# Performance work log

Hardware: AMD Instinct MI355X
Metric: run time of the kernel (lower is better)

## Reference

```python
import jax, jax.numpy as jnp
import numpy as np

B, S, H, NH, K = 8, 1024, 1024, 16, 512
HD = H // NH  # head dim = 64


def setup_inputs() -> dict:
    key = jax.random.key(0)
    ks = jax.random.split(key, 9)
    hidden_states = jax.random.normal(ks[0], (B, S, H), jnp.float32)
    # remain_layers: exactly K nonzero entries per row (static max_tokens = K)
    scores = jax.random.uniform(ks[1], (B, S))
    thresh = jnp.sort(scores, axis=1)[:, S - K][:, None]
    remain_layers = (scores >= thresh).astype(jnp.int32)
    attention_mask = jnp.zeros((B, 1, 1, S), jnp.float32)  # additive mask
    init = 0.02
    Wq = jax.random.normal(ks[2], (H, H), jnp.float32) * init
    bq = jnp.zeros((H,), jnp.float32)
    Wk = jax.random.normal(ks[3], (H, H), jnp.float32) * init
    bk = jnp.zeros((H,), jnp.float32)
    Wv = jax.random.normal(ks[4], (H, H), jnp.float32) * init
    bv = jnp.zeros((H,), jnp.float32)
    return {"hidden_states": hidden_states, "attention_mask": attention_mask,
            "remain_layers": remain_layers, "Wq": Wq, "bq": bq,
            "Wk": Wk, "bk": bk, "Wv": Wv, "bv": bv}


def _heads(x):  # [B, L, H] -> [B, NH, L, HD]
    b, l, _ = x.shape
    return x.reshape(b, l, NH, HD).transpose(0, 2, 1, 3)


def reference(hidden_states, attention_mask, remain_layers, Wq, bq, Wk, bk, Wv, bv):
    # get_reduced_hidden: per-row gather of tokens with remain_layers > 0,
    # in original position order, zero-padded to max_tokens (= K here).
    order = jnp.argsort(1 - remain_layers, axis=1, stable=True)  # nonzeros first, order kept
    idx = order[:, :K]                                           # [B, K]
    reduced = jnp.take_along_axis(hidden_states, idx[:, :, None], axis=1)  # [B, K, H]
    valid = (jnp.take_along_axis(remain_layers, idx, axis=1) > 0)
    reduced = reduced * valid[:, :, None].astype(reduced.dtype)  # zero-pad slots

    q = _heads(reduced @ Wq.T + bq)          # [B, NH, K, HD]
    k = _heads(hidden_states @ Wk.T + bk)    # [B, NH, S, HD]
    v = _heads(hidden_states @ Wv.T + bv)    # [B, NH, S, HD]

    scores = jnp.einsum('bhqd,bhkd->bhqk', q, k) / np.sqrt(HD).astype(np.float32)
    scores = scores + attention_mask         # additive mask broadcast
    probs = jax.nn.softmax(scores, axis=-1)  # dropout is identity at eval
    ctx = jnp.einsum('bhqk,bhkd->bhqd', probs, v)  # [B, NH, K, HD]
    ctx = ctx.transpose(0, 2, 1, 3).reshape(B, K, H)
    return ctx
```

## Files before the change

### kernel.cpp

```cpp
#include <hip/hip_runtime.h>
#include <hip/hip_bf16.h>
#include <stdint.h>

#define S_LEN 1024
#define HDIM  1024
#define NHEADS 16
#define HEAD_D 64
#define KSEL  512
#define BATCH 8

typedef unsigned short ushort_t;
typedef __attribute__((ext_vector_type(8))) __bf16 bf16x8;
typedef __attribute__((ext_vector_type(4))) float  f32x4;
typedef __attribute__((ext_vector_type(16))) float f32x16;

typedef const __attribute__((address_space(1))) void cg_void;
typedef __attribute__((address_space(3))) void lds_void;

__device__ __forceinline__ void gl_lds16(const void* g, void* l) {
    __builtin_amdgcn_global_load_lds((cg_void*)g, (lds_void*)l, 16, 0, 0);
}

__device__ __forceinline__ ushort_t f2bf(float f) {
    union { float f; unsigned int i; } x; x.f = f;
    unsigned int r = (x.i + 0x7fffu + ((x.i >> 16) & 1u)) >> 16;
    return (ushort_t)r;
}

#define BAR() __asm__ volatile("s_barrier" ::: "memory")
#define VMCNT(n) __asm__ volatile("s_waitcnt vmcnt(" #n ")" ::: "memory")
#define LGKM0() __asm__ volatile("s_waitcnt lgkmcnt(0)" ::: "memory")

__global__ __launch_bounds__(1024) void prep_kernel(
    const float* __restrict__ hidden, const float* __restrict__ wq,
    const float* __restrict__ wk, const float* __restrict__ wv,
    const int* __restrict__ remain,
    ushort_t* __restrict__ hbf, ushort_t* __restrict__ wqb,
    ushort_t* __restrict__ wkb, ushort_t* __restrict__ wvb,
    int* __restrict__ idx, int* __restrict__ valid) {
    __shared__ int wsum[16];
    __shared__ int woff[17];
    int blk = blockIdx.x;
    if (blk < 2816) {
        const float* s; ushort_t* d; int base;
        if (blk < 2048)      { s = hidden; d = hbf; base = blk; }
        else if (blk < 2304) { s = wq; d = wqb; base = blk - 2048; }
        else if (blk < 2560) { s = wk; d = wkb; base = blk - 2304; }
        else                 { s = wv; d = wvb; base = blk - 2560; }
        int i = base * 1024 + threadIdx.x;
        float4 v = ((const float4*)s)[i];
        ushort4 o;
        o.x = f2bf(v.x); o.y = f2bf(v.y); o.z = f2bf(v.z); o.w = f2bf(v.w);
        ((ushort4*)d)[i] = o;
    } else {
        int b = blk - 2816, t = threadIdx.x;
        int r = remain[b * S_LEN + t];
        unsigned long long m = __ballot(r != 0);
        int lane = t & 63, w = t >> 6;
        int pre = __popcll(m & ((1ull << lane) - 1ull));
        if (lane == 0) wsum[w] = __popcll(m);
        __syncthreads();
        if (t == 0) { int a = 0; for (int i = 0; i < 16; i++) { woff[i] = a; a += wsum[i]; } woff[16] = a; }
        __syncthreads();
        int tot = woff[16];
        int onesBefore = woff[w] + pre;
        int slot = r ? onesBefore : (tot + (t - onesBefore));
        if (slot < KSEL) { idx[b * KSEL + slot] = t; valid[b * KSEL + slot] = r; }
    }
}

#define QSCALE 0.1803368801111244f
#define LT_PITCH 136
__global__ __launch_bounds__(256, 4) void gemm_fused(
    const ushort_t* __restrict__ hbf, const ushort_t* __restrict__ wkv,
    const ushort_t* __restrict__ wq,
    const float* __restrict__ bk, const float* __restrict__ bv,
    const float* __restrict__ bq,
    const int* __restrict__ idx, const int* __restrict__ valid,
    ushort_t* __restrict__ kp, ushort_t* __restrict__ vt, ushort_t* __restrict__ qp) {
    __shared__ __align__(16) ushort_t pool[16384];
    ushort_t* As = pool;
    ushort_t* Bs = pool + 8192;
    const int i = blockIdx.x;
    int z, bmI, bnI;
    if (i < 256) { z = 1; bmI = i >> 3; bnI = i & 7; }
    else         { z = 0; int ii = i - 256; int x = ii & 7, j = ii >> 3;
                   bmI = x * 8 + (j & 7); bnI = j >> 3; }
    const long bm = (long)bmI * 128;
    const int bn = bnI * 128;

    const int tid = threadIdx.x;
    const int lane = tid & 63;
    const int w = tid >> 6;
    const int quad = lane >> 4;
    const int cl = lane & 15;
    const int srow = w * 16 + (lane >> 2);
    const int fs = ((lane >> 2) & 3) ^ ((lane >> 4) & 3);
    const int scol = ((lane & 3) ^ fs) * 8;
    const int lds_off = w * 512 + lane * 8;
    const int wr = (w >> 1) * 64, wc = (w & 1) * 64;
    const int fr = (cl & 3) ^ ((cl >> 2) & 3);
    const int qo = (quad ^ fr) * 8;

    const ushort_t* W = z ? wq : wkv;

    long ab[2];
#pragma unroll
    for (int p = 0; p < 2; p++) {
        long gr = bm + p * 64 + srow;
        if (z == 0) ab[p] = gr * HDIM;
        else {
            int b_ = (int)(gr >> 9);
            int src = idx[(b_ << 9) + ((int)gr & 511)];
            ab[p] = ((long)(b_ << 10) + src) * HDIM;
        }
    }

    f32x4 acc[4][4] = {};

    for (int k0 = 0; k0 < HDIM; k0 += 64) {
#pragma unroll
        for (int p = 0; p < 2; p++)
#pragma unroll
            for (int hh = 0; hh < 2; hh++) {
                gl_lds16(hbf + ab[p] + k0 + hh * 32 + scol, &As[hh * 4096 + p * 2048 + lds_off]);
                gl_lds16(W + ((long)(bn + p * 64 + srow)) * HDIM + k0 + hh * 32 + scol,
                         &Bs[hh * 4096 + p * 2048 + lds_off]);
            }
        __syncthreads();
#pragma unroll
        for (int hh = 0; hh < 2; hh++) {
            bf16x8 af[4], bfr[4];
#pragma unroll
            for (int mt = 0; mt < 4; mt++)
                af[mt] = *(const bf16x8*)&As[hh * 4096 + (wr + mt * 16 + cl) * 32 + qo];
#pragma unroll
            for (int nt = 0; nt < 4; nt++)
                bfr[nt] = *(const bf16x8*)&Bs[hh * 4096 + (wc + nt * 16 + cl) * 32 + qo];
#pragma unroll
            for (int mt = 0; mt < 4; mt++)
#pragma unroll
                for (int nt = 0; nt < 4; nt++)
                    acc[mt][nt] = __builtin_amdgcn_mfma_f32_16x16x32_bf16(af[mt], bfr[nt], acc[mt][nt], 0, 0, 0);
        }
        __syncthreads();
    }

    if (z == 1) {
#pragma unroll
        for (int nt = 0; nt < 4; nt++) {
            int col = bn + wc + nt * 16 + cl;
            float bvq = bq[col];
#pragma unroll
            for (int mt = 0; mt < 4; mt++) {
                long row = bm + wr + mt * 16 + quad * 4;
#pragma unroll
                for (int r = 0; r < 4; r++) {
                    float vm = (float)valid[row + r];
                    qp[(row + r) * HDIM + col] = f2bf((acc[mt][nt][r] * vm + bvq) * QSCALE);
                }
            }
        }
    } else if (bn < 1024) {
#pragma unroll
        for (int nt = 0; nt < 4; nt++) {
            int col = bn + wc + nt * 16 + cl;
            float bvk = bk[col];
#pragma unroll
            for (int mt = 0; mt < 4; mt++) {
                long row = bm + wr + mt * 16 + quad * 4;
#pragma unroll
                for (int r = 0; r < 4; r++)
                    kp[(row + r) * HDIM + col] = f2bf(acc[mt][nt][r] + bvk);
            }
        }
    } else {
        ushort_t* Lt = pool;
        long b_ = bm >> 10, s0 = bm & 1023;
#pragma unroll
        for (int p2 = 0; p2 < 2; p2++) {
            if ((w & 1) == p2) {
#pragma unroll
                for (int nt = 0; nt < 4; nt++) {
                    int cloc = nt * 16 + cl;
                    float bvv = bv[bn - 1024 + p2 * 64 + cloc];
#pragma unroll
                    for (int mt = 0; mt < 4; mt++) {
                        int row0 = wr + mt * 16 + quad * 4;
#pragma unroll
                        for (int r = 0; r < 4; r++)
                            Lt[cloc * LT_PITCH + row0 + r] = f2bf(acc[mt][nt][r] + bvv);
                    }
                }
            }
            __syncthreads();
            int c2 = tid >> 2, quarter = tid & 3;
            long gbase = ((b_ << 10) + (bn - 1024) + p2 * 64 + c2) * 1024 + s0 + quarter * 32;
            const ushort_t* src = Lt + c2 * LT_PITCH + quarter * 32;
#pragma unroll
            for (int q8 = 0; q8 < 4; q8++)
                *(bf16x8*)(vt + gbase + q8 * 8) = *(const bf16x8*)(src + q8 * 8);
            __syncthreads();
        }
    }
}

__global__ __launch_bounds__(256, 2) void attn_kernel(
    const ushort_t* __restrict__ qp, const ushort_t* __restrict__ kp,
    const ushort_t* __restrict__ vt, const float* __restrict__ mask,
    float* __restrict__ out) {
    __shared__ __align__(16) ushort_t ks[3][4096];
    __shared__ __align__(16) ushort_t vs[3][4096];
    __shared__ float mlds[1024];
    const int tid = threadIdx.x;
    const int lane = tid & 63;
    const int w = tid >> 6;
    const int ql = lane & 31;
    const int hi = lane >> 5;
    const int qt = blockIdx.x, h = blockIdx.y, b = blockIdx.z;

    const int sr2 = tid >> 3;
    const int scS = ((tid & 7) ^ (sr2 & 7)) * 8;
    const int dOf = tid * 8;

    const long kbase = (long)b * S_LEN;
    const long vbase = (long)b * 1024 + h * HEAD_D;

    {
        float4 mv4 = *(const float4*)(mask + b * S_LEN + tid * 4);
        mlds[tid * 4 + 0] = mv4.x * 1.44269504f;
        mlds[tid * 4 + 1] = mv4.y * 1.44269504f;
        mlds[tid * 4 + 2] = mv4.z * 1.44269504f;
        mlds[tid * 4 + 3] = mv4.w * 1.44269504f;
    }

    const long qrow0 = (long)b * KSEL + qt * 128 + w * 32;
    bf16x8 aq[4];
#pragma unroll
    for (int kd = 0; kd < 4; kd++)
        aq[kd] = *(const bf16x8*)(qp + (qrow0 + ql) * HDIM + h * HEAD_D + kd * 16 + hi * 8);

    f32x16 O[2] = {};
    float l_loc = 0.f;

    auto stage = [&](int t, int slot) {
#pragma unroll
        for (int j = 0; j < 2; j++) {
            gl_lds16(kp + (kbase + t * 64 + j * 32 + sr2) * (long)HDIM + h * HEAD_D + scS,
                     &ks[slot][j * 2048 + dOf]);
            gl_lds16(vt + (vbase + j * 32 + sr2) * (long)S_LEN + t * 64 + scS,
                     &vs[slot][j * 2048 + dOf]);
        }
    };

    stage(0, 0);
    stage(1, 1);
    LGKM0();

    int slotC = 0;
    int slotP = 2;
    for (int c = 0; c < S_LEN / 64; c++) {
        BAR();
        if (c + 2 < S_LEN / 64) stage(c + 2, slotP);
        if (c < 14)       { VMCNT(8); }
        else if (c == 14) { VMCNT(4); }
        else              { VMCNT(0); }
        BAR();
        const ushort_t* kb_ = ks[slotC];
        const ushort_t* vb_ = vs[slotC];

        f32x16 sc[2] = {};
        __builtin_amdgcn_s_setprio(1);
#pragma unroll
        for (int kd = 0; kd < 4; kd++)
#pragma unroll
            for (int mtk = 0; mtk < 2; mtk++) {
                int row = mtk * 32 + ql;
                bf16x8 af = *(const bf16x8*)&kb_[row * 64 + (((kd * 2 + hi) ^ (row & 7)) * 8)];
                sc[mtk] = __builtin_amdgcn_mfma_f32_32x32x16_bf16(af, aq[kd], sc[mtk], 0, 0, 0);
            }
        __builtin_amdgcn_s_setprio(0);

#pragma unroll
        for (int mtk = 0; mtk < 2; mtk++)
#pragma unroll
            for (int g = 0; g < 4; g++) {
                f32x4 m4 = *(const f32x4*)&mlds[c * 64 + mtk * 32 + g * 8 + hi * 4];
#pragma unroll
                for (int j = 0; j < 4; j++) {
                    float p_ = __builtin_amdgcn_exp2f(sc[mtk][g * 4 + j] + m4[j]);
                    sc[mtk][g * 4 + j] = p_;
                    l_loc += p_;
                }
            }

        bf16x8 pa[4];
#pragma unroll
        for (int mtk = 0; mtk < 2; mtk++)
#pragma unroll
            for (int sub = 0; sub < 2; sub++) {
                unsigned a0, a1, b0, b1;
                __asm__("v_cvt_pk_bf16_f32 %0, %1, %2" : "=v"(a0)
                        : "v"(sc[mtk][sub * 8 + 0]), "v"(sc[mtk][sub * 8 + 1]));
                __asm__("v_cvt_pk_bf16_f32 %0, %1, %2" : "=v"(a1)
                        : "v"(sc[mtk][sub * 8 + 2]), "v"(sc[mtk][sub * 8 + 3]));
                __asm__("v_cvt_pk_bf16_f32 %0, %1, %2" : "=v"(b0)
                        : "v"(sc[mtk][sub * 8 + 4]), "v"(sc[mtk][sub * 8 + 5]));
                __asm__("v_cvt_pk_bf16_f32 %0, %1, %2" : "=v"(b1)
                        : "v"(sc[mtk][sub * 8 + 6]), "v"(sc[mtk][sub * 8 + 7]));
                __asm__("v_permlane32_swap_b32 %0, %1" : "+v"(a0), "+v"(b0));
                __asm__("v_permlane32_swap_b32 %0, %1" : "+v"(a1), "+v"(b1));
                union { unsigned u[4]; bf16x8 v; } fr;
                fr.u[0] = a0; fr.u[1] = a1; fr.u[2] = b0; fr.u[3] = b1;
                pa[mtk * 2 + sub] = fr.v;
            }

        __builtin_amdgcn_s_setprio(1);
#pragma unroll
        for (int ks_ = 0; ks_ < 4; ks_++)
#pragma unroll
            for (int ntd = 0; ntd < 2; ntd++) {
                int row = ntd * 32 + ql;
                bf16x8 bvf = *(const bf16x8*)&vb_[row * 64 + (((ks_ * 2 + hi) ^ (row & 7)) * 8)];
                O[ntd] = __builtin_amdgcn_mfma_f32_32x32x16_bf16(bvf, pa[ks_], O[ntd], 0, 0, 0);
            }
        __builtin_amdgcn_s_setprio(0);

        slotC = (slotC == 2) ? 0 : slotC + 1;
        slotP = (slotP == 2) ? 0 : slotP + 1;
    }

    l_loc += __shfl_xor(l_loc, 32, 64);

#pragma unroll
    for (int ntd = 0; ntd < 2; ntd++)
#pragma unroll
        for (int g = 0; g < 4; g++) {
            float4 o4;
            o4.x = O[ntd][g * 4 + 0] / l_loc;
            o4.y = O[ntd][g * 4 + 1] / l_loc;
            o4.z = O[ntd][g * 4 + 2] / l_loc;
            o4.w = O[ntd][g * 4 + 3] / l_loc;
            *(float4*)(out + (qrow0 + ql) * HDIM + h * HEAD_D + ntd * 32 + g * 8 + hi * 4) = o4;
        }
}

extern "C" void kernel_launch(void* const* d_in, const int* in_sizes, int n_in,
                              void* d_out, int out_size, void* d_ws, size_t ws_size,
                              hipStream_t stream) {
    const float* hidden = (const float*)d_in[0];
    const float* mask   = (const float*)d_in[1];
    const int*   remain = (const int*)d_in[2];
    const float* Wq = (const float*)d_in[3];
    const float* bq = (const float*)d_in[4];
    const float* Wk = (const float*)d_in[5];
    const float* bk = (const float*)d_in[6];
    const float* Wv = (const float*)d_in[7];
    const float* bv = (const float*)d_in[8];
    float* out = (float*)d_out;

    char* ws = (char*)d_ws;
    size_t off = 0;
    int* idx   = (int*)(ws + off); off += 16384;
    int* valid = (int*)(ws + off); off += 16384;
    ushort_t* hbf = (ushort_t*)(ws + off); off += (size_t)BATCH * S_LEN * HDIM * 2;
    ushort_t* wqb = (ushort_t*)(ws + off); off += (size_t)HDIM * HDIM * 2;
    ushort_t* wkb = (ushort_t*)(ws + off); off += (size_t)HDIM * HDIM * 2;
    ushort_t* wvb = (ushort_t*)(ws + off); off += (size_t)HDIM * HDIM * 2;
    ushort_t* qp  = (ushort_t*)(ws + off); off += (size_t)BATCH * KSEL * HDIM * 2;
    ushort_t* kp  = (ushort_t*)(ws + off); off += (size_t)BATCH * S_LEN * HDIM * 2;
    ushort_t* vt  = (ushort_t*)(ws + off); off += (size_t)BATCH * S_LEN * HDIM * 2;

    prep_kernel<<<2824, 1024, 0, stream>>>(hidden, Wq, Wk, Wv, remain,
                                           hbf, wqb, wkb, wvb, idx, valid);
    gemm_fused<<<1280, 256, 0, stream>>>(hbf, wkb, wqb, bk, bv, bq,
                                         idx, valid, kp, vt, qp);
    attn_kernel<<<dim3(4, NHEADS, BATCH), 256, 0, stream>>>(qp, kp, vt, mask, out);
}
```

Measured before the change: 187.1 us.

## Split fused QKV GEMM into separate launches and remap attention blocks per XCD

The fused Q/K/V projection kernel is split into a dedicated Q GEMM and a K/V GEMM launched in two halves. This removes per-block branching on the Q path and the idx indirection from K/V blocks. The attention grid becomes 1D, with block IDs remapped so that the four query tiles of the same (batch, head) land on the same XCD and share K/V in its L2. The cost is extra kernel launches and smaller grids that may underfill the device.

```diff
diff --git a/kernel.cpp b/kernel.cpp
--- a/kernel.cpp
+++ b/kernel.cpp
@@ -71,21 +71,18 @@
 
 #define QSCALE 0.1803368801111244f
 #define LT_PITCH 136
-__global__ __launch_bounds__(256, 4) void gemm_fused(
+
+__global__ __launch_bounds__(256, 4) void gemm_kv(
     const ushort_t* __restrict__ hbf, const ushort_t* __restrict__ wkv,
-    const ushort_t* __restrict__ wq,
     const float* __restrict__ bk, const float* __restrict__ bv,
-    const float* __restrict__ bq,
-    const int* __restrict__ idx, const int* __restrict__ valid,
-    ushort_t* __restrict__ kp, ushort_t* __restrict__ vt, ushort_t* __restrict__ qp) {
+    ushort_t* __restrict__ kp, ushort_t* __restrict__ vt, int noff) {
     __shared__ __align__(16) ushort_t pool[16384];
     ushort_t* As = pool;
     ushort_t* Bs = pool + 8192;
-    const int i = blockIdx.x;
-    int z, bmI, bnI;
-    if (i < 256) { z = 1; bmI = i >> 3; bnI = i & 7; }
-    else         { z = 0; int ii = i - 256; int x = ii & 7, j = ii >> 3;
-                   bmI = x * 8 + (j & 7); bnI = j >> 3; }
+    const int ii = blockIdx.x + noff;
+    const int x = ii & 7, j = ii >> 3;
+    const int bmI = x * 8 + (j & 7);
+    const int bnI = j >> 3;
     const long bm = (long)bmI * 128;
     const int bn = bnI * 128;
 
@@ -102,20 +99,6 @@
     const int fr = (cl & 3) ^ ((cl >> 2) & 3);
     const int qo = (quad ^ fr) * 8;
 
-    const ushort_t* W = z ? wq : wkv;
-
-    long ab[2];
-#pragma unroll
-    for (int p = 0; p < 2; p++) {
-        long gr = bm + p * 64 + srow;
-        if (z == 0) ab[p] = gr * HDIM;
-        else {
-            int b_ = (int)(gr >> 9);
-            int src = idx[(b_ << 9) + ((int)gr & 511)];
-            ab[p] = ((long)(b_ << 10) + src) * HDIM;
-        }
-    }
-
     f32x4 acc[4][4] = {};
 
     for (int k0 = 0; k0 < HDIM; k0 += 64) {
@@ -123,8 +106,9 @@
         for (int p = 0; p < 2; p++)
 #pragma unroll
             for (int hh = 0; hh < 2; hh++) {
-                gl_lds16(hbf + ab[p] + k0 + hh * 32 + scol, &As[hh * 4096 + p * 2048 + lds_off]);
-                gl_lds16(W + ((long)(bn + p * 64 + srow)) * HDIM + k0 + hh * 32 + scol,
+                gl_lds16(hbf + (bm + p * 64 + srow) * HDIM + k0 + hh * 32 + scol,
+                         &As[hh * 4096 + p * 2048 + lds_off]);
+                gl_lds16(wkv + ((long)(bn + p * 64 + srow)) * HDIM + k0 + hh * 32 + scol,
                          &Bs[hh * 4096 + p * 2048 + lds_off]);
             }
         __syncthreads();
@@ -146,22 +130,7 @@
         __syncthreads();
     }
 
-    if (z == 1) {
-#pragma unroll
-        for (int nt = 0; nt < 4; nt++) {
-            int col = bn + wc + nt * 16 + cl;
-            float bvq = bq[col];
-#pragma unroll
-            for (int mt = 0; mt < 4; mt++) {
-                long row = bm + wr + mt * 16 + quad * 4;
-#pragma unroll
-                for (int r = 0; r < 4; r++) {
-                    float vm = (float)valid[row + r];
-                    qp[(row + r) * HDIM + col] = f2bf((acc[mt][nt][r] * vm + bvq) * QSCALE);
-                }
-            }
-        }
-    } else if (bn < 1024) {
+    if (bn < 1024) {
 #pragma unroll
         for (int nt = 0; nt < 4; nt++) {
             int col = bn + wc + nt * 16 + cl;
@@ -201,6 +170,87 @@
             for (int q8 = 0; q8 < 4; q8++)
                 *(bf16x8*)(vt + gbase + q8 * 8) = *(const bf16x8*)(src + q8 * 8);
             __syncthreads();
+        }
+    }
+}
+
+__global__ __launch_bounds__(256, 4) void gemm_q(
+    const ushort_t* __restrict__ hbf, const ushort_t* __restrict__ wq,
+    const float* __restrict__ bq,
+    const int* __restrict__ idx, const int* __restrict__ valid,
+    ushort_t* __restrict__ qp) {
+    __shared__ __align__(16) ushort_t pool[16384];
+    ushort_t* As = pool;
+    ushort_t* Bs = pool + 8192;
+    const int i = blockIdx.x;
+    const int bmI = i >> 3, bnI = i & 7;
+    const long bm = (long)bmI * 128;
+    const int bn = bnI * 128;
+
+    const int tid = threadIdx.x;
+    const int lane = tid & 63;
+    const int w = tid >> 6;
+    const int quad = lane >> 4;
+    const int cl = lane & 15;
+    const int srow = w * 16 + (lane >> 2);
+    const int fs = ((lane >> 2) & 3) ^ ((lane >> 4) & 3);
+    const int scol = ((lane & 3) ^ fs) * 8;
+    const int lds_off = w * 512 + lane * 8;
+    const int wr = (w >> 1) * 64, wc = (w & 1) * 64;
+    const int fr = (cl & 3) ^ ((cl >> 2) & 3);
+    const int qo = (quad ^ fr) * 8;
+
+    long ab[2];
+#pragma unroll
+    for (int p = 0; p < 2; p++) {
+        long gr = bm + p * 64 + srow;
+        int b_ = (int)(gr >> 9);
+        int src = idx[(b_ << 9) + ((int)gr & 511)];
+        ab[p] = ((long)(b_ << 10) + src) * HDIM;
+    }
+
+    f32x4 acc[4][4] = {};
+
+    for (int k0 = 0; k0 < HDIM; k0 += 64) {
+#pragma unroll
+        for (int p = 0; p < 2; p++)
+#pragma unroll
+            for (int hh = 0; hh < 2; hh++) {
+                gl_lds16(hbf + ab[p] + k0 + hh * 32 + scol, &As[hh * 4096 + p * 2048 + lds_off]);
+                gl_lds16(wq + ((long)(bn + p * 64 + srow)) * HDIM + k0 + hh * 32 + scol,
+                         &Bs[hh * 4096 + p * 2048 + lds_off]);
+            }
+        __syncthreads();
+#pragma unroll
+        for (int hh = 0; hh < 2; hh++) {
+            bf16x8 af[4], bfr[4];
+#pragma unroll
+            for (int mt = 0; mt < 4; mt++)
+                af[mt] = *(const bf16x8*)&As[hh * 4096 + (wr + mt * 16 + cl) * 32 + qo];
+#pragma unroll
+            for (int nt = 0; nt < 4; nt++)
+                bfr[nt] = *(const bf16x8*)&Bs[hh * 4096 + (wc + nt * 16 + cl) * 32 + qo];
+#pragma unroll
+            for (int mt = 0; mt < 4; mt++)
+#pragma unroll
+                for (int nt = 0; nt < 4; nt++)
+                    acc[mt][nt] = __builtin_amdgcn_mfma_f32_16x16x32_bf16(af[mt], bfr[nt], acc[mt][nt], 0, 0, 0);
+        }
+        __syncthreads();
+    }
+
+#pragma unroll
+    for (int nt = 0; nt < 4; nt++) {
+        int col = bn + wc + nt * 16 + cl;
+        float bvq = bq[col];
+#pragma unroll
+        for (int mt = 0; mt < 4; mt++) {
+            long row = bm + wr + mt * 16 + quad * 4;
+#pragma unroll
+            for (int r = 0; r < 4; r++) {
+                float vm = (float)valid[row + r];
+                qp[(row + r) * HDIM + col] = f2bf((acc[mt][nt][r] * vm + bvq) * QSCALE);
+            }
         }
     }
 }
@@ -217,7 +267,13 @@
     const int w = tid >> 6;
     const int ql = lane & 31;
     const int hi = lane >> 5;
-    const int qt = blockIdx.x, h = blockIdx.y, b = blockIdx.z;
+    const int bid = blockIdx.x;
+    const int xcd = bid & 7;
+    const int slot = bid >> 3;
+    const int qt = slot & 3;
+    const int gg = xcd + 8 * (slot >> 2);
+    const int h = gg & 15;
+    const int b = gg >> 4;
 
     const int sr2 = tid >> 3;
     const int scS = ((tid & 7) ^ (sr2 & 7)) * 8;
@@ -243,13 +299,13 @@
     f32x16 O[2] = {};
     float l_loc = 0.f;
 
-    auto stage = [&](int t, int slot) {
+    auto stage = [&](int t, int sl) {
 #pragma unroll
         for (int j = 0; j < 2; j++) {
             gl_lds16(kp + (kbase + t * 64 + j * 32 + sr2) * (long)HDIM + h * HEAD_D + scS,
-                     &ks[slot][j * 2048 + dOf]);
+                     &ks[sl][j * 2048 + dOf]);
             gl_lds16(vt + (vbase + j * 32 + sr2) * (long)S_LEN + t * 64 + scS,
-                     &vs[slot][j * 2048 + dOf]);
+                     &vs[sl][j * 2048 + dOf]);
         }
     };
 
@@ -373,7 +429,8 @@
 
     prep_kernel<<<2824, 1024, 0, stream>>>(hidden, Wq, Wk, Wv, remain,
                                            hbf, wqb, wkb, wvb, idx, valid);
-    gemm_fused<<<1280, 256, 0, stream>>>(hbf, wkb, wqb, bk, bv, bq,
-                                         idx, valid, kp, vt, qp);
-    attn_kernel<<<dim3(4, NHEADS, BATCH), 256, 0, stream>>>(qp, kp, vt, mask, out);
-}
+    gemm_q<<<256, 256, 0, stream>>>(hbf, wqb, bq, idx, valid, qp);
+    gemm_kv<<<512, 256, 0, stream>>>(hbf, wkb, bk, bv, kp, vt, 0);
+    gemm_kv<<<512, 256, 0, stream>>>(hbf, wkb, bk, bv, kp, vt, 512);
+    attn_kernel<<<512, 256, 0, stream>>>(qp, kp, vt, mask, out);
+}
```

After: 197.7 us. 5.7% more time.
